# Kernel tuning notes

Measured on AMD Instinct MI355X. Metric: run time of the kernel, lower is better.

## Reference

```python
import jax, jax.numpy as jnp
import numpy as np

N, E, F = 50000, 500000, 32
H, C = 4, 64          # nheads, graph_hidden_channels
NHID, NOUT, B = 256, 256, 1000


def setup_inputs() -> dict:
    key = jax.random.key(0)
    ks = jax.random.split(key, 24)
    s = 0.05
    inp = {
        "x": jax.random.normal(ks[0], (N, F), jnp.float32),
        "edge_index": jax.random.randint(ks[1], (2, E), 0, N, jnp.int64),
        "batch": jnp.sort(jax.random.randint(ks[2], (N,), 0, B, jnp.int64)),
        # conv1: F -> H*C
        "W1": jax.random.normal(ks[3], (F, H * C), jnp.float32) * s,
        "a_src1": jax.random.normal(ks[4], (H, C), jnp.float32) * s,
        "a_dst1": jax.random.normal(ks[5], (H, C), jnp.float32) * s,
        "b1": jnp.zeros((H * C,), jnp.float32),
        # conv2: H*C -> H*C
        "W2": jax.random.normal(ks[6], (H * C, H * C), jnp.float32) * s,
        "a_src2": jax.random.normal(ks[7], (H, C), jnp.float32) * s,
        "a_dst2": jax.random.normal(ks[8], (H, C), jnp.float32) * s,
        "b2": jnp.zeros((H * C,), jnp.float32),
        # conv3: H*C -> C, heads=1
        "W3": jax.random.normal(ks[9], (H * C, C), jnp.float32) * s,
        "a_src3": jax.random.normal(ks[10], (1, C), jnp.float32) * s,
        "a_dst3": jax.random.normal(ks[11], (1, C), jnp.float32) * s,
        "b3": jnp.zeros((C,), jnp.float32),
        # MLP head + LayerNorm
        "Wm1": jax.random.normal(ks[12], (C, NHID), jnp.float32) * s,
        "bm1": jnp.zeros((NHID,), jnp.float32),
        "Wm2": jax.random.normal(ks[13], (NHID, NOUT), jnp.float32) * s,
        "bm2": jnp.zeros((NOUT,), jnp.float32),
        "g2": jnp.ones((NOUT,), jnp.float32),
        "be2": jnp.zeros((NOUT,), jnp.float32),
    }
    return inp


def _gat_conv(x, ei, W, a_src, a_dst, bias, heads, ch):
    """PyG GATConv: linear -> per-edge leaky_relu attention -> segment softmax
    over incoming edges of each dst node -> scatter-add aggregation."""
    n = x.shape[0]
    h = (x @ W).reshape(n, heads, ch)                     # [N,H,C]
    src, dst = ei[0], ei[1]
    al_s = jnp.sum(h * a_src, axis=-1)                    # [N,H]
    al_d = jnp.sum(h * a_dst, axis=-1)                    # [N,H]
    e = jax.nn.leaky_relu(al_s[src] + al_d[dst], 0.2)     # [E,H]
    m = jax.ops.segment_max(e, dst, num_segments=n)       # stable softmax
    p = jnp.exp(e - m[dst])
    z = jax.ops.segment_sum(p, dst, num_segments=n)
    alpha = p / (z[dst] + 1e-16)                          # [E,H]
    out = jax.ops.segment_sum(alpha[:, :, None] * h[src], dst, num_segments=n)
    return out.reshape(n, heads * ch) + bias


def _layer_norm(x, g, b, eps=1e-5):
    mu = jnp.mean(x, axis=-1, keepdims=True)
    v = jnp.var(x, axis=-1, keepdims=True)
    return (x - mu) * jax.lax.rsqrt(v + eps) * g + b


def reference(x, edge_index, batch, W1, a_src1, a_dst1, b1, W2, a_src2, a_dst2, b2,
              W3, a_src3, a_dst3, b3, Wm1, bm1, Wm2, bm2, g2, be2):
    n = x.shape[0]
    loops = jnp.tile(jnp.arange(n, dtype=edge_index.dtype)[None, :], (2, 1))
    ei = jnp.concatenate([edge_index, loops], axis=1)     # add_self_loops=True
    h1 = jax.nn.relu(_gat_conv(x, ei, W1, a_src1, a_dst1, b1, H, C))
    h2 = jax.nn.relu(_gat_conv(h1, ei, W2, a_src2, a_dst2, b2, H, C))
    h3 = _gat_conv(h2, ei, W3, a_src3, a_dst3, b3, 1, C)  # [N,C]
    cnt = jax.ops.segment_sum(jnp.ones((n,), h3.dtype), batch, num_segments=B)
    xg = jax.ops.segment_sum(h3, batch, num_segments=B) / jnp.maximum(cnt, 1.0)[:, None]
    y = jax.nn.relu(xg @ Wm1 + bm1)
    y = y @ Wm2 + bm2
    return _layer_norm(y, g2, be2)
```

## Files before the change

### kernel.cpp

```cpp
#include <hip/hip_runtime.h>
#include <hip/hip_bf16.h>

#define N_NODES 50000
#define N_PAD 50176
#define N_EDGES 500000
#define E2_EDGES 550000
#define F_IN 32
#define HEADS 4
#define CH 64
#define HC 256
#define NB 1000
#define NHID 256
#define NOUT 256
#define SLOT_CAP 64

static inline int cdiv(long long a, long long b) { return (int)((a + b - 1) / b); }

typedef __bf16 bf16x8 __attribute__((ext_vector_type(8)));
typedef unsigned short us8 __attribute__((ext_vector_type(8)));
typedef unsigned short us4 __attribute__((ext_vector_type(4)));
typedef float f32x4 __attribute__((ext_vector_type(4)));
union BU { us8 u; bf16x8 b; };

__device__ inline unsigned short f2bf(float f) {
    unsigned u = __float_as_uint(f);
    return (unsigned short)((u + 0x7fffu + ((u >> 16) & 1u)) >> 16);
}
__device__ inline float bf2f(unsigned short h) {
    return __uint_as_float(((unsigned)h) << 16);
}

__device__ inline void wconv_one(const float* __restrict__ W,
                                 unsigned short* __restrict__ Wf_hi,
                                 unsigned short* __restrict__ Wf_lo,
                                 int K, int M, int idx) {
    int k = idx / M, m = idx % M;
    float v = W[idx];
    unsigned short hi = f2bf(v);
    unsigned short lo = f2bf(v - bf2f(hi));
    int tcol = m >> 4, l16 = m & 15;
    int ch = k >> 5, quad = (k >> 3) & 3, j = k & 7;
    int NCH = K >> 5;
    size_t dst = ((((size_t)tcol * NCH + ch) * 64) + quad * 16 + l16) * 8 + j;
    Wf_hi[dst] = hi;
    Wf_lo[dst] = lo;
}

#define PREP_T0 N_NODES
#define PREP_T1 (PREP_T0 + N_NODES * F_IN)
#define PREP_T2 (PREP_T1 + F_IN * HC)
#define PREP_T3 (PREP_T2 + HC * HC)
#define PREP_T4 (PREP_T3 + HC * CH)
__global__ void prep_kernel(const float* __restrict__ x,
                            unsigned short* __restrict__ xh,
                            unsigned short* __restrict__ xl,
                            const float* __restrict__ W1,
                            unsigned short* __restrict__ wt1h, unsigned short* __restrict__ wt1l,
                            const float* __restrict__ W2,
                            unsigned short* __restrict__ wt2h, unsigned short* __restrict__ wt2l,
                            const float* __restrict__ W3,
                            unsigned short* __restrict__ wt3h, unsigned short* __restrict__ wt3l,
                            int* __restrict__ deg) {
    int t = blockIdx.x * blockDim.x + threadIdx.x;
    if (t < PREP_T0) {
        deg[t] = 0;
    } else if (t < PREP_T1) {
        int i = t - PREP_T0;
        int node = i / F_IN, c = i % F_IN;
        float v = x[i];
        unsigned short hi = f2bf(v);
        size_t dst = (((size_t)(node >> 4)) * 64 + ((c >> 3) & 3) * 16 + (node & 15)) * 8 + (c & 7);
        xh[dst] = hi;
        xl[dst] = f2bf(v - bf2f(hi));
    } else if (t < PREP_T2) {
        wconv_one(W1, wt1h, wt1l, F_IN, HC, t - PREP_T1);
    } else if (t < PREP_T3) {
        wconv_one(W2, wt2h, wt2l, HC, HC, t - PREP_T2);
    } else if (t < PREP_T4) {
        wconv_one(W3, wt3h, wt3l, HC, CH, t - PREP_T3);
    }
}

__global__ void scatter_kernel(const int* __restrict__ ei, int* __restrict__ deg,
                               unsigned short* __restrict__ slots) {
    int e = blockIdx.x * blockDim.x + threadIdx.x;
    if (e >= E2_EDGES) return;
    int s, d;
    if (e < N_EDGES) { s = ei[e]; d = ei[N_EDGES + e]; }
    else             { s = d = e - N_EDGES; }
    int pos = atomicAdd(deg + d, 1);
    if (pos < SLOT_CAP) slots[(d << 6) + pos] = (unsigned short)s;
}

template<int K, int M, bool ALO>
__global__ __launch_bounds__(256) void mfma_lin_fused_kernel(
    const unsigned short* __restrict__ Ah, const unsigned short* __restrict__ Al,
    const unsigned short* __restrict__ Wf_hi, const unsigned short* __restrict__ Wf_lo,
    const float* __restrict__ a_src, const float* __restrict__ a_dst,
    unsigned short* __restrict__ Hout, float* __restrict__ als,
    float* __restrict__ ald, int n_rows) {
    constexpr int NCH = K / 32;
    constexpr int CW = M / 64;
    constexpr int RW = 4 / CW;
    constexpr int H_ = M / 64;
    const int wave = threadIdx.x >> 6, lane = threadIdx.x & 63;
    const int quad = lane >> 4, l16 = lane & 15;
    const int head = wave % CW;
    const int col0 = head * 64;
    const int row0 = blockIdx.x * (RW * 64) + (wave / CW) * 64;
    const int rt0 = row0 >> 4;

    f32x4 acc[4][4];
#pragma unroll
    for (int rs = 0; rs < 4; rs++)
#pragma unroll
        for (int t = 0; t < 4; t++) acc[rs][t] = (f32x4){0.f, 0.f, 0.f, 0.f};

    const unsigned short* aph[4];
    const unsigned short* apl[4];
#pragma unroll
    for (int rs = 0; rs < 4; rs++) {
        size_t off = (((size_t)(rt0 + rs) * NCH) * 64 + lane) * 8;
        aph[rs] = Ah + off;
        if (ALO) apl[rs] = Al + off;
    }
    const unsigned short* bh = Wf_hi + ((size_t)(col0 >> 4) * NCH * 64 + lane) * 8;
    const unsigned short* bl = Wf_lo + ((size_t)(col0 >> 4) * NCH * 64 + lane) * 8;

#pragma unroll
    for (int ch = 0; ch < NCH; ch++) {
        BU a_h[4], a_l[4], b_h[4], b_l[4];
#pragma unroll
        for (int rs = 0; rs < 4; rs++) {
            a_h[rs].u = *(const us8*)(aph[rs] + ch * 512);
            if (ALO) a_l[rs].u = *(const us8*)(apl[rs] + ch * 512);
        }
#pragma unroll
        for (int t = 0; t < 4; t++) {
            b_h[t].u = *(const us8*)(bh + (size_t)(t * NCH + ch) * 512);
            b_l[t].u = *(const us8*)(bl + (size_t)(t * NCH + ch) * 512);
        }
#pragma unroll
        for (int t = 0; t < 4; t++) {
#pragma unroll
            for (int rs = 0; rs < 4; rs++) {
                acc[rs][t] = __builtin_amdgcn_mfma_f32_16x16x32_bf16(a_h[rs].b, b_h[t].b, acc[rs][t], 0, 0, 0);
                acc[rs][t] = __builtin_amdgcn_mfma_f32_16x16x32_bf16(a_h[rs].b, b_l[t].b, acc[rs][t], 0, 0, 0);
                if (ALO)
                    acc[rs][t] = __builtin_amdgcn_mfma_f32_16x16x32_bf16(a_l[rs].b, b_h[t].b, acc[rs][t], 0, 0, 0);
            }
        }
    }

    float sv[4], dv[4];
#pragma unroll
    for (int t = 0; t < 4; t++) {
        sv[t] = a_src[col0 + t * 16 + l16];
        dv[t] = a_dst[col0 + t * 16 + l16];
    }
#pragma unroll
    for (int rs = 0; rs < 4; rs++) {
        const int orow0 = row0 + rs * 16 + quad * 4;
#pragma unroll
        for (int i = 0; i < 4; i++) {
            int r = orow0 + i;
            bool ok = (r < n_rows);
            float ps = 0.f, pd = 0.f;
#pragma unroll
            for (int t = 0; t < 4; t++) {
                float v = acc[rs][t][i];
                ps += v * sv[t];
                pd += v * dv[t];
                if (ok) Hout[(size_t)r * M + col0 + t * 16 + l16] = f2bf(v);
            }
            ps += __shfl_xor(ps, 1);  pd += __shfl_xor(pd, 1);
            ps += __shfl_xor(ps, 2);  pd += __shfl_xor(pd, 2);
            ps += __shfl_xor(ps, 4);  pd += __shfl_xor(pd, 4);
            ps += __shfl_xor(ps, 8);  pd += __shfl_xor(pd, 8);
            if (l16 == 0 && ok) {
                als[r * H_ + head] = ps;
                ald[r * H_ + head] = pd;
            }
        }
    }
}

__global__ __launch_bounds__(256, 4) void gat_agg_v3_kernel(
    const unsigned short* __restrict__ slots, const int* __restrict__ deg,
    const unsigned short* __restrict__ h,
    const float* __restrict__ als, const float* __restrict__ ald,
    const float* __restrict__ bias, unsigned short* __restrict__ outh) {
    constexpr int LP = 264;
    __shared__ unsigned short smh[16 * LP];
    const int tid = threadIdx.x;
    const int wave = tid >> 6, lane = tid & 63;
    const int cl = lane & 31, half = lane >> 5;
    const int head = cl >> 3;
    const int rt = blockIdx.x;

    float bv[8];
#pragma unroll
    for (int i = 0; i < 8; i++) bv[i] = bias[cl * 8 + i];

    const int nb = rt * 16 + wave * 4;
    int lenv[4];
    float adv[4];
#pragma unroll
    for (int nn = 0; nn < 4; nn++) {
        lenv[nn] = min(deg[nb + nn], SLOT_CAP);
        adv[nn] = ald[((nb + nn) << 2) + head];
    }
    const unsigned short* hp = h + cl * 8;

    for (int nn = 0; nn < 4; nn++) {
        const int len = lenv[nn];
        const int lm = len - 1;
        const int base = (nb + nn) << 6;
        const float ad = adv[nn];
        float z = 0.f;
        float a[8];
#pragma unroll
        for (int i = 0; i < 8; i++) a[i] = 0.f;
        for (int k = 0; k < len; k += 16) {
            int ss[8];
#pragma unroll
            for (int j = 0; j < 8; j++) {
                int ii = min(k + 2 * j + half, lm);
                ss[j] = (int)slots[base + ii];
            }
            __builtin_amdgcn_sched_barrier(0);
            us8 hv[8];
            float alv[8];
#pragma unroll
            for (int j = 0; j < 8; j++) {
                hv[j] = *(const us8*)(hp + ((size_t)ss[j] << 8));
                alv[j] = als[(ss[j] << 2) + head];
            }
            __builtin_amdgcn_sched_barrier(0);
            float p[8];
#pragma unroll
            for (int j = 0; j < 8; j++) {
                float x = alv[j] + ad;
                x = (x > 0.f) ? x : 0.2f * x;
                int e = k + 2 * j + half;
                p[j] = (e < len) ? __expf(x) : 0.f;
                z += p[j];
            }
#pragma unroll
            for (int j = 0; j < 8; j++)
#pragma unroll
                for (int i = 0; i < 8; i++)
                    a[i] += p[j] * bf2f(hv[j][i]);
        }
        z += __shfl_xor(z, 32);
#pragma unroll
        for (int i = 0; i < 8; i++) a[i] += __shfl_xor(a[i], 32);
        if (half == 0) {
            float inv = 1.f / (z + 1e-16f);
            us8 vh;
#pragma unroll
            for (int i = 0; i < 8; i++) {
                float v = fmaxf(a[i] * inv + bv[i], 0.f);
                vh[i] = f2bf(v);
            }
            int nl = wave * 4 + nn;
            *(us8*)(smh + nl * LP + cl * 8) = vh;
        }
    }
    __syncthreads();
#pragma unroll
    for (int f = tid; f < 512; f += 256) {
        int chunk = f >> 6, ln2 = f & 63;
        int quad = ln2 >> 4, l16 = ln2 & 15;
        us8 vh = *(const us8*)(smh + l16 * LP + chunk * 32 + quad * 8);
        size_t dst = (((size_t)rt * 8 + chunk) * 64 + ln2) * 8;
        *(us8*)(outh + dst) = vh;
    }
}

__global__ __launch_bounds__(256) void gat_agg_h1_kernel(
    const unsigned short* __restrict__ slots, const int* __restrict__ deg,
    const unsigned short* __restrict__ h,
    const float* __restrict__ als, const float* __restrict__ ald,
    const float* __restrict__ bias, float* __restrict__ out, int n) {
    const int wave = threadIdx.x >> 6, lane = threadIdx.x & 63;
    const int eg = lane >> 3, cg = lane & 7;
    const int node = (blockIdx.x << 2) + wave;
    if (node >= n) return;
    const int base = node << 6;
    const int len = min(deg[node], SLOT_CAP);
    const float ad = ald[node];
    float z = 0.f;
    float a[8];
#pragma unroll
    for (int i = 0; i < 8; i++) a[i] = 0.f;
    const unsigned short* hp = h + cg * 8;
    for (int k = 0; k < len; k += 8) {
        int e = k + eg;
        int s0 = (int)slots[base + min(e, len - 1)];
        us8 hv = *(const us8*)(hp + ((size_t)s0 << 6));
        float x = als[s0] + ad;
        x = (x > 0.f) ? x : 0.2f * x;
        float p = (e < len) ? __expf(x) : 0.f;
        z += p;
#pragma unroll
        for (int i = 0; i < 8; i++) a[i] += p * bf2f(hv[i]);
    }
#pragma unroll
    for (int off = 8; off <= 32; off <<= 1) {
        z += __shfl_xor(z, off);
#pragma unroll
        for (int i = 0; i < 8; i++) a[i] += __shfl_xor(a[i], off);
    }
    if (eg == 0) {
        float inv = 1.f / (z + 1e-16f);
        float* op = out + ((size_t)node << 6) + cg * 8;
        float4 o0, o1;
        o0.x = a[0] * inv + bias[cg * 8 + 0];
        o0.y = a[1] * inv + bias[cg * 8 + 1];
        o0.z = a[2] * inv + bias[cg * 8 + 2];
        o0.w = a[3] * inv + bias[cg * 8 + 3];
        o1.x = a[4] * inv + bias[cg * 8 + 4];
        o1.y = a[5] * inv + bias[cg * 8 + 5];
        o1.z = a[6] * inv + bias[cg * 8 + 6];
        o1.w = a[7] * inv + bias[cg * 8 + 7];
        *(float4*)op = o0;
        *(float4*)(op + 4) = o1;
    }
}

__global__ __launch_bounds__(256) void head_fused_kernel(
    const float* __restrict__ h3, const int* __restrict__ batch,
    const float* __restrict__ Wm1, const float* __restrict__ bm1,
    const float* __restrict__ Wm2, const float* __restrict__ bm2,
    const float* __restrict__ g2, const float* __restrict__ be2,
    float* __restrict__ out) {
    const int b = blockIdx.x;
    const int tid = threadIdx.x;
    int lo = 0, hi = N_NODES;
    while (lo < hi) { int mid = (lo + hi) >> 1; if (batch[mid] < b) lo = mid + 1; else hi = mid; }
    const int start = lo;
    hi = N_NODES;
    while (lo < hi) { int mid = (lo + hi) >> 1; if (batch[mid] < b + 1) lo = mid + 1; else hi = mid; }
    const int end = lo;

    __shared__ float pr[4][CH];
    __shared__ float xg[CH];
    __shared__ float yr[NHID];
    const int j = tid & 63, g = tid >> 6;
    float s = 0.f;
    for (int n = start + g; n < end; n += 4) s += h3[(size_t)n * CH + j];
    pr[g][j] = s;
    __syncthreads();
    if (tid < CH) {
        float t = pr[0][tid] + pr[1][tid] + pr[2][tid] + pr[3][tid];
        xg[tid] = t / fmaxf((float)(end - start), 1.f);
    }
    __syncthreads();
    float acc1 = bm1[tid];
#pragma unroll 8
    for (int k = 0; k < CH; k++) acc1 += xg[k] * Wm1[(size_t)k * NHID + tid];
    yr[tid] = fmaxf(acc1, 0.f);
    __syncthreads();
    float acc = bm2[tid];
#pragma unroll 8
    for (int k = 0; k < NHID; k++) acc += yr[k] * Wm2[(size_t)k * NOUT + tid];
    float ss = acc, s2 = acc * acc;
    for (int o = 32; o > 0; o >>= 1) {
        ss += __shfl_down(ss, o);
        s2 += __shfl_down(s2, o);
    }
    __shared__ float red[8];
    __shared__ float mv[2];
    int wave = tid >> 6, lane = tid & 63;
    if (lane == 0) { red[wave] = ss; red[4 + wave] = s2; }
    __syncthreads();
    if (tid == 0) {
        float ts = red[0] + red[1] + red[2] + red[3];
        float ts2 = red[4] + red[5] + red[6] + red[7];
        float mu = ts / (float)NOUT;
        float var = ts2 / (float)NOUT - mu * mu;
        mv[0] = mu;
        mv[1] = rsqrtf(var + 1e-5f);
    }
    __syncthreads();
    out[(size_t)b * NOUT + tid] = (acc - mv[0]) * mv[1] * g2[tid] + be2[tid];
}

extern "C" void kernel_launch(void* const* d_in, const int* in_sizes, int n_in,
                              void* d_out, int out_size, void* d_ws, size_t ws_size,
                              hipStream_t stream) {
    const float* x      = (const float*)d_in[0];
    const int*   ei     = (const int*)d_in[1];
    const int*   batch  = (const int*)d_in[2];
    const float* W1     = (const float*)d_in[3];
    const float* as1    = (const float*)d_in[4];
    const float* ad1    = (const float*)d_in[5];
    const float* b1     = (const float*)d_in[6];
    const float* W2     = (const float*)d_in[7];
    const float* as2    = (const float*)d_in[8];
    const float* ad2    = (const float*)d_in[9];
    const float* b2     = (const float*)d_in[10];
    const float* W3     = (const float*)d_in[11];
    const float* as3    = (const float*)d_in[12];
    const float* ad3    = (const float*)d_in[13];
    const float* b3     = (const float*)d_in[14];
    const float* Wm1    = (const float*)d_in[15];
    const float* bm1    = (const float*)d_in[16];
    const float* Wm2    = (const float*)d_in[17];
    const float* bm2    = (const float*)d_in[18];
    const float* g2     = (const float*)d_in[19];
    const float* be2    = (const float*)d_in[20];
    float* out = (float*)d_out;

    unsigned short* bufH = (unsigned short*)d_ws;
    unsigned short* aggh = bufH + (size_t)N_NODES * HC;
    unsigned short* xh   = aggh + (size_t)N_PAD * HC;
    unsigned short* xl   = xh + (size_t)N_PAD * F_IN;
    unsigned short* slots = xh;
    float* bufO3 = (float*)(xl + (size_t)N_PAD * F_IN);
    float* als   = bufO3 + (size_t)N_NODES * CH;
    float* ald   = als + (size_t)N_NODES * HEADS;
    int* deg     = (int*)(ald + (size_t)N_NODES * HEADS);
    unsigned short* wt1h = (unsigned short*)(deg + N_NODES);
    unsigned short* wt1l = wt1h + 256 * 32;
    unsigned short* wt2h = wt1l + 256 * 32;
    unsigned short* wt2l = wt2h + 256 * 256;
    unsigned short* wt3h = wt2l + 256 * 256;
    unsigned short* wt3l = wt3h + 64 * 256;

    const int BLK = 256;

    prep_kernel<<<cdiv(PREP_T4, BLK), BLK, 0, stream>>>(
        x, xh, xl, W1, wt1h, wt1l, W2, wt2h, wt2l, W3, wt3h, wt3l, deg);

    mfma_lin_fused_kernel<F_IN, HC, true><<<cdiv(N_NODES, 64), 256, 0, stream>>>(
        xh, xl, wt1h, wt1l, as1, ad1, bufH, als, ald, N_NODES);

    scatter_kernel<<<cdiv(E2_EDGES, BLK), BLK, 0, stream>>>(ei, deg, slots);

    gat_agg_v3_kernel<<<N_NODES / 16, 256, 0, stream>>>(
        slots, deg, bufH, als, ald, b1, aggh);

    mfma_lin_fused_kernel<HC, HC, false><<<cdiv(N_NODES, 64), 256, 0, stream>>>(
        aggh, nullptr, wt2h, wt2l, as2, ad2, bufH, als, ald, N_NODES);
    gat_agg_v3_kernel<<<N_NODES / 16, 256, 0, stream>>>(
        slots, deg, bufH, als, ald, b2, aggh);

    mfma_lin_fused_kernel<HC, CH, false><<<cdiv(N_NODES, 256), 256, 0, stream>>>(
        aggh, nullptr, wt3h, wt3l, as3, ad3, bufH, als, ald, N_NODES);
    gat_agg_h1_kernel<<<cdiv(N_NODES, 4), 256, 0, stream>>>(
        slots, deg, bufH, als, ald, b3, bufO3, N_NODES);

    head_fused_kernel<<<NB, 256, 0, stream>>>(
        bufO3, batch, Wm1, bm1, Wm2, bm2, g2, be2, out);
}
```

Measured before the change: 324.7 us.

## Fuse all GAT stages into one persistent cooperative kernel with grid syncs

Replaces the chain of separate launches for the GEMMs, scatter, aggregation and MLP head with a single cooperative persistent kernel. Blocks pull tiles from per-phase atomic counters and separate phases with grid.sync(). The goal is to remove per-launch overhead and tail gaps between the eight kernels. In exchange, the occupancy cap of 3 blocks per CU constrains the register-heavy GEMM and aggregation tiles, and each grid barrier has its own cost; the old multi-launch path is kept as a fallback.

```diff
diff --git a/kernel.cpp b/kernel.cpp
--- a/kernel.cpp
+++ b/kernel.cpp
@@ -1,5 +1,8 @@
 #include <hip/hip_runtime.h>
 #include <hip/hip_bf16.h>
+#include <hip/hip_cooperative_groups.h>
+
+namespace cg = cooperative_groups;
 
 #define N_NODES 50000
 #define N_PAD 50176
@@ -18,7 +21,6 @@
 
 typedef __bf16 bf16x8 __attribute__((ext_vector_type(8)));
 typedef unsigned short us8 __attribute__((ext_vector_type(8)));
-typedef unsigned short us4 __attribute__((ext_vector_type(4)));
 typedef float f32x4 __attribute__((ext_vector_type(4)));
 union BU { us8 u; bf16x8 b; };
 
@@ -60,8 +62,9 @@
                             unsigned short* __restrict__ wt2h, unsigned short* __restrict__ wt2l,
                             const float* __restrict__ W3,
                             unsigned short* __restrict__ wt3h, unsigned short* __restrict__ wt3l,
-                            int* __restrict__ deg) {
+                            int* __restrict__ deg, int* __restrict__ ctrs) {
     int t = blockIdx.x * blockDim.x + threadIdx.x;
+    if (t < 8) ctrs[t] = 0;
     if (t < PREP_T0) {
         deg[t] = 0;
     } else if (t < PREP_T1) {
@@ -81,9 +84,11 @@
     }
 }
 
-__global__ void scatter_kernel(const int* __restrict__ ei, int* __restrict__ deg,
-                               unsigned short* __restrict__ slots) {
-    int e = blockIdx.x * blockDim.x + threadIdx.x;
+
+__device__ __forceinline__ void scatter_tile(int t, const int* __restrict__ ei,
+                                             int* __restrict__ deg,
+                                             unsigned short* __restrict__ slots) {
+    int e = t * 256 + threadIdx.x;
     if (e >= E2_EDGES) return;
     int s, d;
     if (e < N_EDGES) { s = ei[e]; d = ei[N_EDGES + e]; }
@@ -93,7 +98,8 @@
 }
 
 template<int K, int M, bool ALO>
-__global__ __launch_bounds__(256) void mfma_lin_fused_kernel(
+__device__ __forceinline__ void gemm_tile(
+    int bid,
     const unsigned short* __restrict__ Ah, const unsigned short* __restrict__ Al,
     const unsigned short* __restrict__ Wf_hi, const unsigned short* __restrict__ Wf_lo,
     const float* __restrict__ a_src, const float* __restrict__ a_dst,
@@ -107,7 +113,7 @@
     const int quad = lane >> 4, l16 = lane & 15;
     const int head = wave % CW;
     const int col0 = head * 64;
-    const int row0 = blockIdx.x * (RW * 64) + (wave / CW) * 64;
+    const int row0 = bid * (RW * 64) + (wave / CW) * 64;
     const int rt0 = row0 >> 4;
 
     f32x4 acc[4][4];
@@ -185,18 +191,18 @@
     }
 }
 
-__global__ __launch_bounds__(256, 4) void gat_agg_v3_kernel(
+#define AGG_LP 264
+
+__device__ __forceinline__ void agg_tile(
+    int rt, unsigned short* smh,
     const unsigned short* __restrict__ slots, const int* __restrict__ deg,
     const unsigned short* __restrict__ h,
     const float* __restrict__ als, const float* __restrict__ ald,
     const float* __restrict__ bias, unsigned short* __restrict__ outh) {
-    constexpr int LP = 264;
-    __shared__ unsigned short smh[16 * LP];
     const int tid = threadIdx.x;
     const int wave = tid >> 6, lane = tid & 63;
     const int cl = lane & 31, half = lane >> 5;
     const int head = cl >> 3;
-    const int rt = blockIdx.x;
 
     float bv[8];
 #pragma unroll
@@ -264,7 +270,7 @@
                 vh[i] = f2bf(v);
             }
             int nl = wave * 4 + nn;
-            *(us8*)(smh + nl * LP + cl * 8) = vh;
+            *(us8*)(smh + nl * AGG_LP + cl * 8) = vh;
         }
     }
     __syncthreads();
@@ -272,20 +278,20 @@
     for (int f = tid; f < 512; f += 256) {
         int chunk = f >> 6, ln2 = f & 63;
         int quad = ln2 >> 4, l16 = ln2 & 15;
-        us8 vh = *(const us8*)(smh + l16 * LP + chunk * 32 + quad * 8);
+        us8 vh = *(const us8*)(smh + l16 * AGG_LP + chunk * 32 + quad * 8);
         size_t dst = (((size_t)rt * 8 + chunk) * 64 + ln2) * 8;
         *(us8*)(outh + dst) = vh;
     }
 }
 
-__global__ __launch_bounds__(256) void gat_agg_h1_kernel(
-    const unsigned short* __restrict__ slots, const int* __restrict__ deg,
+__device__ __forceinline__ void agg_h1_tile(
+    int t, const unsigned short* __restrict__ slots, const int* __restrict__ deg,
     const unsigned short* __restrict__ h,
     const float* __restrict__ als, const float* __restrict__ ald,
     const float* __restrict__ bias, float* __restrict__ out, int n) {
     const int wave = threadIdx.x >> 6, lane = threadIdx.x & 63;
     const int eg = lane >> 3, cg = lane & 7;
-    const int node = (blockIdx.x << 2) + wave;
+    const int node = (t << 2) + wave;
     if (node >= n) return;
     const int base = node << 6;
     const int len = min(deg[node], SLOT_CAP);
@@ -329,13 +335,18 @@
     }
 }
 
-__global__ __launch_bounds__(256) void head_fused_kernel(
+__device__ __forceinline__ void head_tile(
+    int b, float* sm,
     const float* __restrict__ h3, const int* __restrict__ batch,
     const float* __restrict__ Wm1, const float* __restrict__ bm1,
     const float* __restrict__ Wm2, const float* __restrict__ bm2,
     const float* __restrict__ g2, const float* __restrict__ be2,
     float* __restrict__ out) {
-    const int b = blockIdx.x;
+    float* pr = sm;
+    float* xg = sm + 256;
+    float* yr = sm + 320;
+    float* red = sm + 576;
+    float* mv = sm + 584;
     const int tid = threadIdx.x;
     int lo = 0, hi = N_NODES;
     while (lo < hi) { int mid = (lo + hi) >> 1; if (batch[mid] < b) lo = mid + 1; else hi = mid; }
@@ -344,16 +355,13 @@
     while (lo < hi) { int mid = (lo + hi) >> 1; if (batch[mid] < b + 1) lo = mid + 1; else hi = mid; }
     const int end = lo;
 
-    __shared__ float pr[4][CH];
-    __shared__ float xg[CH];
-    __shared__ float yr[NHID];
     const int j = tid & 63, g = tid >> 6;
     float s = 0.f;
     for (int n = start + g; n < end; n += 4) s += h3[(size_t)n * CH + j];
-    pr[g][j] = s;
+    pr[g * 64 + j] = s;
     __syncthreads();
     if (tid < CH) {
-        float t = pr[0][tid] + pr[1][tid] + pr[2][tid] + pr[3][tid];
+        float t = pr[tid] + pr[64 + tid] + pr[128 + tid] + pr[192 + tid];
         xg[tid] = t / fmaxf((float)(end - start), 1.f);
     }
     __syncthreads();
@@ -370,8 +378,6 @@
         ss += __shfl_down(ss, o);
         s2 += __shfl_down(s2, o);
     }
-    __shared__ float red[8];
-    __shared__ float mv[2];
     int wave = tid >> 6, lane = tid & 63;
     if (lane == 0) { red[wave] = ss; red[4 + wave] = s2; }
     __syncthreads();
@@ -385,6 +391,107 @@
     }
     __syncthreads();
     out[(size_t)b * NOUT + tid] = (acc - mv[0]) * mv[1] * g2[tid] + be2[tid];
+    __syncthreads();
+}
+
+struct MegaArgs {
+    const unsigned short *xh, *xl;
+    const unsigned short *wt1h, *wt1l, *wt2h, *wt2l, *wt3h, *wt3l;
+    const float *as1, *ad1, *b1;
+    const float *as2, *ad2, *b2;
+    const float *as3, *ad3, *b3;
+    const float *Wm1, *bm1, *Wm2, *bm2, *g2, *be2;
+    const int *ei, *batch;
+    unsigned short *slots;
+    int *deg;
+    unsigned short *bufH, *aggh;
+    float *bufO3, *als, *ald, *out;
+    int *ctrs;
+};
+
+#define NT_G12 ((N_NODES + 63) / 64)
+#define NT_SC  ((E2_EDGES + 255) / 256)
+#define NT_AG  (N_NODES / 16)
+#define NT_G3  ((N_NODES + 255) / 256)
+#define NT_H1  (N_NODES / 4)
+
+#define RUN_PHASE(ph, NT, CALL)                                  \
+    while (true) {                                               \
+        __syncthreads();                                         \
+        if (tid == 0) s_t = atomicAdd(&A.ctrs[ph], 1);           \
+        __syncthreads();                                         \
+        int t = s_t;                                             \
+        if (t >= (NT)) break;                                    \
+        CALL;                                                    \
+    }                                                            \
+    grid.sync();
+
+__global__ __launch_bounds__(256, 3) void mega_kernel(MegaArgs A) {
+    cg::grid_group grid = cg::this_grid();
+    __shared__ __align__(16) unsigned short smh[16 * AGG_LP];
+    __shared__ int s_t;
+    const int tid = threadIdx.x;
+
+    RUN_PHASE(0, NT_G12, (gemm_tile<F_IN, HC, true>(t, A.xh, A.xl, A.wt1h, A.wt1l,
+                           A.as1, A.ad1, A.bufH, A.als, A.ald, N_NODES)));
+    RUN_PHASE(1, NT_SC, (scatter_tile(t, A.ei, A.deg, A.slots)));
+    RUN_PHASE(2, NT_AG, (agg_tile(t, smh, A.slots, A.deg, A.bufH, A.als, A.ald, A.b1, A.aggh)));
+    RUN_PHASE(3, NT_G12, (gemm_tile<HC, HC, false>(t, A.aggh, nullptr, A.wt2h, A.wt2l,
+                           A.as2, A.ad2, A.bufH, A.als, A.ald, N_NODES)));
+    RUN_PHASE(4, NT_AG, (agg_tile(t, smh, A.slots, A.deg, A.bufH, A.als, A.ald, A.b2, A.aggh)));
+    RUN_PHASE(5, NT_G3, (gemm_tile<HC, CH, false>(t, A.aggh, nullptr, A.wt3h, A.wt3l,
+                           A.as3, A.ad3, A.bufH, A.als, A.ald, N_NODES)));
+    RUN_PHASE(6, NT_H1, (agg_h1_tile(t, A.slots, A.deg, A.bufH, A.als, A.ald, A.b3, A.bufO3, N_NODES)));
+    while (true) {
+        __syncthreads();
+        if (tid == 0) s_t = atomicAdd(&A.ctrs[7], 1);
+        __syncthreads();
+        int t = s_t;
+        if (t >= NB) break;
+        head_tile(t, (float*)smh, A.bufO3, A.batch, A.Wm1, A.bm1, A.Wm2, A.bm2, A.g2, A.be2, A.out);
+    }
+}
+
+__global__ void scatter_kernel(const int* __restrict__ ei, int* __restrict__ deg,
+                               unsigned short* __restrict__ slots) {
+    scatter_tile(blockIdx.x, ei, deg, slots);
+}
+
+template<int K, int M, bool ALO>
+__global__ __launch_bounds__(256) void mfma_lin_fused_kernel(
+    const unsigned short* __restrict__ Ah, const unsigned short* __restrict__ Al,
+    const unsigned short* __restrict__ Wf_hi, const unsigned short* __restrict__ Wf_lo,
+    const float* __restrict__ a_src, const float* __restrict__ a_dst,
+    unsigned short* __restrict__ Hout, float* __restrict__ als,
+    float* __restrict__ ald, int n_rows) {
+    gemm_tile<K, M, ALO>(blockIdx.x, Ah, Al, Wf_hi, Wf_lo, a_src, a_dst, Hout, als, ald, n_rows);
+}
+
+__global__ __launch_bounds__(256, 4) void gat_agg_v3_kernel(
+    const unsigned short* __restrict__ slots, const int* __restrict__ deg,
+    const unsigned short* __restrict__ h,
+    const float* __restrict__ als, const float* __restrict__ ald,
+    const float* __restrict__ bias, unsigned short* __restrict__ outh) {
+    __shared__ __align__(16) unsigned short smh[16 * AGG_LP];
+    agg_tile(blockIdx.x, smh, slots, deg, h, als, ald, bias, outh);
+}
+
+__global__ __launch_bounds__(256) void gat_agg_h1_kernel(
+    const unsigned short* __restrict__ slots, const int* __restrict__ deg,
+    const unsigned short* __restrict__ h,
+    const float* __restrict__ als, const float* __restrict__ ald,
+    const float* __restrict__ bias, float* __restrict__ out, int n) {
+    agg_h1_tile(blockIdx.x, slots, deg, h, als, ald, bias, out, n);
+}
+
+__global__ __launch_bounds__(256) void head_fused_kernel(
+    const float* __restrict__ h3, const int* __restrict__ batch,
+    const float* __restrict__ Wm1, const float* __restrict__ bm1,
+    const float* __restrict__ Wm2, const float* __restrict__ bm2,
+    const float* __restrict__ g2, const float* __restrict__ be2,
+    float* __restrict__ out) {
+    __shared__ __align__(16) float hsm[592];
+    head_tile(blockIdx.x, hsm, h3, batch, Wm1, bm1, Wm2, bm2, g2, be2, out);
 }
 
 extern "C" void kernel_launch(void* const* d_in, const int* in_sizes, int n_in,
@@ -428,30 +535,73 @@
     unsigned short* wt2l = wt2h + 256 * 256;
     unsigned short* wt3h = wt2l + 256 * 256;
     unsigned short* wt3l = wt3h + 64 * 256;
+    int* ctrs    = (int*)(wt3l + 64 * 256);
 
     const int BLK = 256;
 
     prep_kernel<<<cdiv(PREP_T4, BLK), BLK, 0, stream>>>(
-        x, xh, xl, W1, wt1h, wt1l, W2, wt2h, wt2l, W3, wt3h, wt3l, deg);
-
-    mfma_lin_fused_kernel<F_IN, HC, true><<<cdiv(N_NODES, 64), 256, 0, stream>>>(
-        xh, xl, wt1h, wt1l, as1, ad1, bufH, als, ald, N_NODES);
-
-    scatter_kernel<<<cdiv(E2_EDGES, BLK), BLK, 0, stream>>>(ei, deg, slots);
-
-    gat_agg_v3_kernel<<<N_NODES / 16, 256, 0, stream>>>(
-        slots, deg, bufH, als, ald, b1, aggh);
-
-    mfma_lin_fused_kernel<HC, HC, false><<<cdiv(N_NODES, 64), 256, 0, stream>>>(
-        aggh, nullptr, wt2h, wt2l, as2, ad2, bufH, als, ald, N_NODES);
-    gat_agg_v3_kernel<<<N_NODES / 16, 256, 0, stream>>>(
-        slots, deg, bufH, als, ald, b2, aggh);
-
-    mfma_lin_fused_kernel<HC, CH, false><<<cdiv(N_NODES, 256), 256, 0, stream>>>(
-        aggh, nullptr, wt3h, wt3l, as3, ad3, bufH, als, ald, N_NODES);
-    gat_agg_h1_kernel<<<cdiv(N_NODES, 4), 256, 0, stream>>>(
-        slots, deg, bufH, als, ald, b3, bufO3, N_NODES);
-
-    head_fused_kernel<<<NB, 256, 0, stream>>>(
-        bufO3, batch, Wm1, bm1, Wm2, bm2, g2, be2, out);
-}
+        x, xh, xl, W1, wt1h, wt1l, W2, wt2h, wt2l, W3, wt3h, wt3l, deg, ctrs);
+
+    static int g_mega_grid = -2;
+    if (g_mega_grid == -2) {
+        int nb = 0;
+        hipError_t e1 = hipOccupancyMaxActiveBlocksPerMultiprocessor(
+            &nb, (const void*)mega_kernel, 256, 0);
+        hipDeviceProp_t prop;
+        hipError_t e2 = hipGetDeviceProperties(&prop, 0);
+        if (e1 == hipSuccess && e2 == hipSuccess && nb > 0) {
+            long long g = (long long)nb * prop.multiProcessorCount;
+            if (g > 2048) g = 2048;
+            g_mega_grid = (int)g;
+        } else {
+            g_mega_grid = -1;
+            (void)hipGetLastError();
+        }
+    }
+
+    bool coop_done = false;
+    if (g_mega_grid > 0) {
+        MegaArgs margs;
+        margs.xh = xh; margs.xl = xl;
+        margs.wt1h = wt1h; margs.wt1l = wt1l;
+        margs.wt2h = wt2h; margs.wt2l = wt2l;
+        margs.wt3h = wt3h; margs.wt3l = wt3l;
+        margs.as1 = as1; margs.ad1 = ad1; margs.b1 = b1;
+        margs.as2 = as2; margs.ad2 = ad2; margs.b2 = b2;
+        margs.as3 = as3; margs.ad3 = ad3; margs.b3 = b3;
+        margs.Wm1 = Wm1; margs.bm1 = bm1; margs.Wm2 = Wm2; margs.bm2 = bm2;
+        margs.g2 = g2; margs.be2 = be2;
+        margs.ei = ei; margs.batch = batch;
+        margs.slots = slots; margs.deg = deg;
+        margs.bufH = bufH; margs.aggh = aggh;
+        margs.bufO3 = bufO3; margs.als = als; margs.ald = ald;
+        margs.out = out; margs.ctrs = ctrs;
+        void* kargs[] = { &margs };
+        hipError_t err = hipLaunchCooperativeKernel(
+            (const void*)mega_kernel, dim3(g_mega_grid), dim3(256), kargs, 0, stream);
+        if (err == hipSuccess) {
+            coop_done = true;
+        } else {
+            (void)hipGetLastError();
+            g_mega_grid = -1;
+        }
+    }
+
+    if (!coop_done) {
+        mfma_lin_fused_kernel<F_IN, HC, true><<<cdiv(N_NODES, 64), 256, 0, stream>>>(
+            xh, xl, wt1h, wt1l, as1, ad1, bufH, als, ald, N_NODES);
+        scatter_kernel<<<cdiv(E2_EDGES, BLK), BLK, 0, stream>>>(ei, deg, slots);
+        gat_agg_v3_kernel<<<N_NODES / 16, 256, 0, stream>>>(
+            slots, deg, bufH, als, ald, b1, aggh);
+        mfma_lin_fused_kernel<HC, HC, false><<<cdiv(N_NODES, 64), 256, 0, stream>>>(
+            aggh, nullptr, wt2h, wt2l, as2, ad2, bufH, als, ald, N_NODES);
+        gat_agg_v3_kernel<<<N_NODES / 16, 256, 0, stream>>>(
+            slots, deg, bufH, als, ald, b2, aggh);
+        mfma_lin_fused_kernel<HC, CH, false><<<cdiv(N_NODES, 256), 256, 0, stream>>>(
+            aggh, nullptr, wt3h, wt3l, as3, ad3, bufH, als, ald, N_NODES);
+        gat_agg_h1_kernel<<<cdiv(N_NODES, 4), 256, 0, stream>>>(
+            slots, deg, bufH, als, ald, b3, bufO3, N_NODES);
+        head_fused_kernel<<<NB, 256, 0, stream>>>(
+            bufO3, batch, Wm1, bm1, Wm2, bm2, g2, be2, out);
+    }
+}
```

Result: slower. 926.6 us (+185.4%).

## Merge layer-1 GEMM with edge scatter; fuse graph mean-pool into final aggregation

Applied to the files above, without the earlier changes.

Layer-1 GEMM tiles and the edge-scatter CSR build now run as one launch, with blocks split by index, so they can overlap and one launch is saved. The slots buffer moves to its own workspace region because it can no longer alias the xh input that the GEMM reads in the same launch. The last GAT aggregation now atomically adds each node's output into per-graph sums instead of writing the N×64 h3 tensor, and the head kernel just reads those sums. This removes an intermediate write and read and a launch, but adds float atomics (contention on shared graph rows, nondeterministic summation order).

```diff
diff --git a/kernel.cpp b/kernel.cpp
--- a/kernel.cpp
+++ b/kernel.cpp
@@ -18,7 +18,6 @@
 
 typedef __bf16 bf16x8 __attribute__((ext_vector_type(8)));
 typedef unsigned short us8 __attribute__((ext_vector_type(8)));
-typedef unsigned short us4 __attribute__((ext_vector_type(4)));
 typedef float f32x4 __attribute__((ext_vector_type(4)));
 union BU { us8 u; bf16x8 b; };
 
@@ -47,7 +46,8 @@
 }
 
 #define PREP_T0 N_NODES
-#define PREP_T1 (PREP_T0 + N_NODES * F_IN)
+#define PREP_TG (PREP_T0 + NB * CH)
+#define PREP_T1 (PREP_TG + N_NODES * F_IN)
 #define PREP_T2 (PREP_T1 + F_IN * HC)
 #define PREP_T3 (PREP_T2 + HC * HC)
 #define PREP_T4 (PREP_T3 + HC * CH)
@@ -60,12 +60,14 @@
                             unsigned short* __restrict__ wt2h, unsigned short* __restrict__ wt2l,
                             const float* __restrict__ W3,
                             unsigned short* __restrict__ wt3h, unsigned short* __restrict__ wt3l,
-                            int* __restrict__ deg) {
+                            int* __restrict__ deg, float* __restrict__ xgsum) {
     int t = blockIdx.x * blockDim.x + threadIdx.x;
     if (t < PREP_T0) {
         deg[t] = 0;
+    } else if (t < PREP_TG) {
+        xgsum[t - PREP_T0] = 0.f;
     } else if (t < PREP_T1) {
-        int i = t - PREP_T0;
+        int i = t - PREP_TG;
         int node = i / F_IN, c = i % F_IN;
         float v = x[i];
         unsigned short hi = f2bf(v);
@@ -81,9 +83,11 @@
     }
 }
 
-__global__ void scatter_kernel(const int* __restrict__ ei, int* __restrict__ deg,
-                               unsigned short* __restrict__ slots) {
-    int e = blockIdx.x * blockDim.x + threadIdx.x;
+
+__device__ __forceinline__ void scatter_tile(int t, const int* __restrict__ ei,
+                                             int* __restrict__ deg,
+                                             unsigned short* __restrict__ slots) {
+    int e = t * 256 + threadIdx.x;
     if (e >= E2_EDGES) return;
     int s, d;
     if (e < N_EDGES) { s = ei[e]; d = ei[N_EDGES + e]; }
@@ -93,7 +97,8 @@
 }
 
 template<int K, int M, bool ALO>
-__global__ __launch_bounds__(256) void mfma_lin_fused_kernel(
+__device__ __forceinline__ void gemm_tile(
+    int bid,
     const unsigned short* __restrict__ Ah, const unsigned short* __restrict__ Al,
     const unsigned short* __restrict__ Wf_hi, const unsigned short* __restrict__ Wf_lo,
     const float* __restrict__ a_src, const float* __restrict__ a_dst,
@@ -107,7 +112,7 @@
     const int quad = lane >> 4, l16 = lane & 15;
     const int head = wave % CW;
     const int col0 = head * 64;
-    const int row0 = blockIdx.x * (RW * 64) + (wave / CW) * 64;
+    const int row0 = bid * (RW * 64) + (wave / CW) * 64;
     const int rt0 = row0 >> 4;
 
     f32x4 acc[4][4];
@@ -183,6 +188,34 @@
             }
         }
     }
+}
+
+#define NT_G1 ((N_NODES + 63) / 64)
+#define NT_SC ((E2_EDGES + 255) / 256)
+
+__global__ __launch_bounds__(256) void gemm1_scatter_kernel(
+    const unsigned short* __restrict__ Ah, const unsigned short* __restrict__ Al,
+    const unsigned short* __restrict__ Wf_hi, const unsigned short* __restrict__ Wf_lo,
+    const float* __restrict__ a_src, const float* __restrict__ a_dst,
+    unsigned short* __restrict__ Hout, float* __restrict__ als,
+    float* __restrict__ ald,
+    const int* __restrict__ ei, int* __restrict__ deg,
+    unsigned short* __restrict__ slots) {
+    if (blockIdx.x < NT_G1)
+        gemm_tile<F_IN, HC, true>(blockIdx.x, Ah, Al, Wf_hi, Wf_lo, a_src, a_dst,
+                                  Hout, als, ald, N_NODES);
+    else
+        scatter_tile(blockIdx.x - NT_G1, ei, deg, slots);
+}
+
+template<int K, int M, bool ALO>
+__global__ __launch_bounds__(256) void mfma_lin_fused_kernel(
+    const unsigned short* __restrict__ Ah, const unsigned short* __restrict__ Al,
+    const unsigned short* __restrict__ Wf_hi, const unsigned short* __restrict__ Wf_lo,
+    const float* __restrict__ a_src, const float* __restrict__ a_dst,
+    unsigned short* __restrict__ Hout, float* __restrict__ als,
+    float* __restrict__ ald, int n_rows) {
+    gemm_tile<K, M, ALO>(blockIdx.x, Ah, Al, Wf_hi, Wf_lo, a_src, a_dst, Hout, als, ald, n_rows);
 }
 
 __global__ __launch_bounds__(256, 4) void gat_agg_v3_kernel(
@@ -282,7 +315,8 @@
     const unsigned short* __restrict__ slots, const int* __restrict__ deg,
     const unsigned short* __restrict__ h,
     const float* __restrict__ als, const float* __restrict__ ald,
-    const float* __restrict__ bias, float* __restrict__ out, int n) {
+    const float* __restrict__ bias, const int* __restrict__ batch,
+    float* __restrict__ xgsum, int n) {
     const int wave = threadIdx.x >> 6, lane = threadIdx.x & 63;
     const int eg = lane >> 3, cg = lane & 7;
     const int node = (blockIdx.x << 2) + wave;
@@ -314,23 +348,15 @@
     }
     if (eg == 0) {
         float inv = 1.f / (z + 1e-16f);
-        float* op = out + ((size_t)node << 6) + cg * 8;
-        float4 o0, o1;
-        o0.x = a[0] * inv + bias[cg * 8 + 0];
-        o0.y = a[1] * inv + bias[cg * 8 + 1];
-        o0.z = a[2] * inv + bias[cg * 8 + 2];
-        o0.w = a[3] * inv + bias[cg * 8 + 3];
-        o1.x = a[4] * inv + bias[cg * 8 + 4];
-        o1.y = a[5] * inv + bias[cg * 8 + 5];
-        o1.z = a[6] * inv + bias[cg * 8 + 6];
-        o1.w = a[7] * inv + bias[cg * 8 + 7];
-        *(float4*)op = o0;
-        *(float4*)(op + 4) = o1;
+        float* gp = xgsum + (size_t)batch[node] * CH + cg * 8;
+#pragma unroll
+        for (int i = 0; i < 8; i++)
+            atomicAdd(gp + i, a[i] * inv + bias[cg * 8 + i]);
     }
 }
 
 __global__ __launch_bounds__(256) void head_fused_kernel(
-    const float* __restrict__ h3, const int* __restrict__ batch,
+    const float* __restrict__ xgsum, const int* __restrict__ batch,
     const float* __restrict__ Wm1, const float* __restrict__ bm1,
     const float* __restrict__ Wm2, const float* __restrict__ bm2,
     const float* __restrict__ g2, const float* __restrict__ be2,
@@ -342,20 +368,13 @@
     const int start = lo;
     hi = N_NODES;
     while (lo < hi) { int mid = (lo + hi) >> 1; if (batch[mid] < b + 1) lo = mid + 1; else hi = mid; }
-    const int end = lo;
-
-    __shared__ float pr[4][CH];
+    const int cnt = lo - start;
+
     __shared__ float xg[CH];
     __shared__ float yr[NHID];
-    const int j = tid & 63, g = tid >> 6;
-    float s = 0.f;
-    for (int n = start + g; n < end; n += 4) s += h3[(size_t)n * CH + j];
-    pr[g][j] = s;
-    __syncthreads();
-    if (tid < CH) {
-        float t = pr[0][tid] + pr[1][tid] + pr[2][tid] + pr[3][tid];
-        xg[tid] = t / fmaxf((float)(end - start), 1.f);
-    }
+    __shared__ float red[8];
+    __shared__ float mv[2];
+    if (tid < CH) xg[tid] = xgsum[(size_t)b * CH + tid] / fmaxf((float)cnt, 1.f);
     __syncthreads();
     float acc1 = bm1[tid];
 #pragma unroll 8
@@ -370,8 +389,6 @@
         ss += __shfl_down(ss, o);
         s2 += __shfl_down(s2, o);
     }
-    __shared__ float red[8];
-    __shared__ float mv[2];
     int wave = tid >> 6, lane = tid & 63;
     if (lane == 0) { red[wave] = ss; red[4 + wave] = s2; }
     __syncthreads();
@@ -417,11 +434,11 @@
     unsigned short* aggh = bufH + (size_t)N_NODES * HC;
     unsigned short* xh   = aggh + (size_t)N_PAD * HC;
     unsigned short* xl   = xh + (size_t)N_PAD * F_IN;
-    unsigned short* slots = xh;
-    float* bufO3 = (float*)(xl + (size_t)N_PAD * F_IN);
-    float* als   = bufO3 + (size_t)N_NODES * CH;
+    unsigned short* slots = xl + (size_t)N_PAD * F_IN;
+    float* als   = (float*)(slots + (size_t)N_NODES * SLOT_CAP);
     float* ald   = als + (size_t)N_NODES * HEADS;
-    int* deg     = (int*)(ald + (size_t)N_NODES * HEADS);
+    float* xgsum = ald + (size_t)N_NODES * HEADS;
+    int* deg     = (int*)(xgsum + (size_t)NB * CH);
     unsigned short* wt1h = (unsigned short*)(deg + N_NODES);
     unsigned short* wt1l = wt1h + 256 * 32;
     unsigned short* wt2h = wt1l + 256 * 32;
@@ -432,12 +449,10 @@
     const int BLK = 256;
 
     prep_kernel<<<cdiv(PREP_T4, BLK), BLK, 0, stream>>>(
-        x, xh, xl, W1, wt1h, wt1l, W2, wt2h, wt2l, W3, wt3h, wt3l, deg);
-
-    mfma_lin_fused_kernel<F_IN, HC, true><<<cdiv(N_NODES, 64), 256, 0, stream>>>(
-        xh, xl, wt1h, wt1l, as1, ad1, bufH, als, ald, N_NODES);
-
-    scatter_kernel<<<cdiv(E2_EDGES, BLK), BLK, 0, stream>>>(ei, deg, slots);
+        x, xh, xl, W1, wt1h, wt1l, W2, wt2h, wt2l, W3, wt3h, wt3l, deg, xgsum);
+
+    gemm1_scatter_kernel<<<NT_G1 + NT_SC, 256, 0, stream>>>(
+        xh, xl, wt1h, wt1l, as1, ad1, bufH, als, ald, ei, deg, slots);
 
     gat_agg_v3_kernel<<<N_NODES / 16, 256, 0, stream>>>(
         slots, deg, bufH, als, ald, b1, aggh);
@@ -450,8 +465,8 @@
     mfma_lin_fused_kernel<HC, CH, false><<<cdiv(N_NODES, 256), 256, 0, stream>>>(
         aggh, nullptr, wt3h, wt3l, as3, ad3, bufH, als, ald, N_NODES);
     gat_agg_h1_kernel<<<cdiv(N_NODES, 4), 256, 0, stream>>>(
-        slots, deg, bufH, als, ald, b3, bufO3, N_NODES);
+        slots, deg, bufH, als, ald, b3, batch, xgsum, N_NODES);
 
     head_fused_kernel<<<NB, 256, 0, stream>>>(
-        bufO3, batch, Wm1, bm1, Wm2, bm2, g2, be2, out);
-}
+        xgsum, batch, Wm1, bm1, Wm2, bm2, g2, be2, out);
+}
```

New measurement: 410.3 us. 1.26x slower.
